# Kernel optimization log

Hardware: AMD Instinct MI355X
Metric: run time of the kernel (lower is better)

Reference implementation:

```python
import jax, jax.numpy as jnp
import numpy as np

N = 100000   # nodes
E = 1600000  # edges (avg degree 16)
DIM = 128    # feature dim
EPS = 1e-6
NEG_SLOPE = 0.2  # tf.nn.leaky_relu default alpha


def layernorm(x, g, b):
    m = jnp.mean(x, axis=-1, keepdims=True)
    v = jnp.mean(jnp.square(x - m), axis=-1, keepdims=True)
    return g * (x - m) * jax.lax.rsqrt(v + EPS) + b


def setup_inputs() -> dict:
    key = jax.random.key(0)
    ks = jax.random.split(key, 12)
    s = 1.0 / np.sqrt(DIM)
    return {
        "query": jax.random.normal(ks[0], (N, DIM), jnp.float32),
        "adj_val": jax.random.uniform(ks[1], (E,), jnp.float32),
        "w_W": jax.random.normal(ks[2], (DIM, DIM), jnp.float32) * s,
        "w_b": jnp.zeros((DIM,), jnp.float32),
        "w1_W": jax.random.normal(ks[3], (DIM, DIM), jnp.float32) * s,
        "w1_b": jnp.zeros((DIM,), jnp.float32),
        "w2_W": jax.random.normal(ks[4], (DIM, DIM), jnp.float32) * s,
        "w2_b": jnp.zeros((DIM,), jnp.float32),
        "ln1_g": jnp.ones((DIM,), jnp.float32),
        "ln1_b": jnp.zeros((DIM,), jnp.float32),
        "ln2_g": jnp.ones((DIM,), jnp.float32),
        "ln2_b": jnp.zeros((DIM,), jnp.float32),
        "adj_row": jnp.sort(jax.random.randint(ks[5], (E,), 0, N, jnp.int32)),
        "adj_col": jax.random.randint(ks[6], (E,), 0, N, jnp.int32),
    }


def reference(query, adj_val, w_W, w_b, w1_W, w1_b, w2_W, w2_b,
              ln1_g, ln1_b, ln2_g, ln2_b, adj_row, adj_col):
    q = layernorm(query, ln1_g, ln1_b)          # [N, D]
    k = q                                        # key is None -> key = query
    value = k @ w_W + w_b                        # [N, D]

    # per-node scalar scores (mean_sum=False branch); dropout in eval mode (identity)
    sum1 = jnp.tanh(jnp.sum(q @ w1_W + w1_b, axis=1))   # [N]
    sum2 = jnp.tanh(jnp.sum(k @ w2_W + w2_b, axis=1))   # [N]

    # sparse add of col-scaled and row-scaled adjacency, then leaky_relu
    logits = jax.nn.leaky_relu(
        adj_val * sum1[adj_row] + adj_val * sum2[adj_col], NEG_SLOPE)  # [E]

    # sparse row-wise softmax over nonzeros
    row_max = jax.ops.segment_max(logits, adj_row, num_segments=N)
    ex = jnp.exp(logits - row_max[adj_row])
    row_sum = jax.ops.segment_sum(ex, adj_row, num_segments=N)
    attn = ex / row_sum[adj_row]                 # [E]

    # spmm: out[i] = sum_e attn[e] * value[col[e]]
    out = jax.ops.segment_sum(attn[:, None] * value[adj_col], adj_row,
                              num_segments=N)    # [N, D]
    return layernorm(out, ln2_g, ln2_b)
```

## Files before the change

### kernel.cpp

```cpp
#include <hip/hip_runtime.h>
#include <hip/hip_bf16.h>

typedef __attribute__((ext_vector_type(8))) short short8;
typedef __attribute__((ext_vector_type(8))) unsigned short ushort8;
typedef __attribute__((ext_vector_type(4))) float f32x4;
typedef __attribute__((ext_vector_type(2))) float f32x2;
typedef __attribute__((ext_vector_type(4))) unsigned int uint4v;

#define DIM 128
#define EPS 1e-6f

__device__ __forceinline__ float wave_sum(float v){
  #pragma unroll
  for (int m = 32; m >= 1; m >>= 1) v += __shfl_xor(v, m);
  return v;
}

__global__ void setup_kernel(const float* __restrict__ w_W,
                             const float* __restrict__ w1_W, const float* __restrict__ w1_b,
                             const float* __restrict__ w2_W, const float* __restrict__ w2_b,
                             __hip_bfloat16* __restrict__ wt_bf,
                             float* __restrict__ u1, float* __restrict__ u2,
                             float* __restrict__ c12){
  const int b = blockIdx.x, tid = threadIdx.x;
  if (b == 0){
    if (tid < DIM){
      float s1 = 0.f, s2 = 0.f;
      for (int j = 0; j < DIM; ++j){ s1 += w1_W[tid*DIM + j]; s2 += w2_W[tid*DIM + j]; }
      u1[tid] = s1; u2[tid] = s2;
    }
    if (tid < 64){
      float c1 = w1_b[tid] + w1_b[tid + 64];
      float c2 = w2_b[tid] + w2_b[tid + 64];
      c1 = wave_sum(c1); c2 = wave_sum(c2);
      if (tid == 0){ c12[0] = c1; c12[1] = c2; }
    }
  } else {
    int idx = (b - 1) * 256 + tid;
    int j = idx >> 7, d = idx & 127;
    wt_bf[idx] = __float2bfloat16(w_W[d*DIM + j]);
  }
}

__launch_bounds__(256)
__global__ void node_kernel(const float* __restrict__ query,
                            const __hip_bfloat16* __restrict__ wt_bf,
                            const float* __restrict__ w_b,
                            const float* __restrict__ ln1_g, const float* __restrict__ ln1_b,
                            const float* __restrict__ u1, const float* __restrict__ u2,
                            const float* __restrict__ c12,
                            unsigned char* __restrict__ value_q,
                            float* __restrict__ sum1, float2* __restrict__ s2v, int N){
  __shared__ __hip_bfloat16 A[64][136];
  const int tid  = threadIdx.x;
  const int lane = tid & 63;
  const int w    = tid >> 6;
  const int q16  = lane >> 4;
  const int lq   = lane & 15;
  const int base = blockIdx.x * 64;

  float uu1[8], uu2[8], gg[8], bv[8];
  {
    const float* p1 = u1 + lq*8; const float* p2 = u2 + lq*8;
    const float* pg = ln1_g + lq*8; const float* pb = ln1_b + lq*8;
    #pragma unroll
    for (int j = 0; j < 8; ++j){ uu1[j]=p1[j]; uu2[j]=p2[j]; gg[j]=pg[j]; bv[j]=pb[j]; }
  }
  const float c1 = c12[0], c2 = c12[1];

  #pragma unroll
  for (int it = 0; it < 4; ++it){
    const int row = w*16 + it*4 + q16;
    const int n   = base + row;
    float x[8];
    if (n < N){
      const float* qp = query + (size_t)n*DIM + lq*8;
      #pragma unroll
      for (int j = 0; j < 8; ++j) x[j] = qp[j];
    } else {
      #pragma unroll
      for (int j = 0; j < 8; ++j) x[j] = 0.f;
    }
    float s = 0.f, s2 = 0.f;
    #pragma unroll
    for (int j = 0; j < 8; ++j){ s += x[j]; s2 += x[j]*x[j]; }
    #pragma unroll
    for (int m = 1; m <= 8; m <<= 1){ s += __shfl_xor(s, m); s2 += __shfl_xor(s2, m); }
    const float mean = s * (1.f/128.f);
    const float var  = s2 * (1.f/128.f) - mean*mean;
    const float rs   = rsqrtf(var + EPS);

    float p1 = 0.f, p2 = 0.f;
    unsigned pk[4];
    #pragma unroll
    for (int j = 0; j < 4; ++j){
      float n0 = gg[2*j]   * (x[2*j]   - mean) * rs + bv[2*j];
      float n1 = gg[2*j+1] * (x[2*j+1] - mean) * rs + bv[2*j+1];
      p1 += n0*uu1[2*j] + n1*uu1[2*j+1];
      p2 += n0*uu2[2*j] + n1*uu2[2*j+1];
      union { __hip_bfloat16 h; unsigned short u; } a_, b_;
      a_.h = __float2bfloat16(n0); b_.h = __float2bfloat16(n1);
      pk[j] = ((unsigned)b_.u << 16) | (unsigned)a_.u;
    }
    uint4v pv = { pk[0], pk[1], pk[2], pk[3] };
    *(uint4v*)&A[row][lq*8] = pv;
    #pragma unroll
    for (int m = 1; m <= 8; m <<= 1){ p1 += __shfl_xor(p1, m); p2 += __shfl_xor(p2, m); }
    if (lq == 0 && n < N){
      sum1[n]   = tanhf(p1 + c1);
      s2v[n].x  = tanhf(p2 + c2);
    }
  }
  __syncthreads();

  const int rh = (w & 1) * 32;
  const int ch = (w >> 1) * 64;
  short8 afr[2][4];
  #pragma unroll
  for (int m = 0; m < 2; ++m)
    #pragma unroll
    for (int ks = 0; ks < 4; ++ks)
      afr[m][ks] = *(const short8*)&A[rh + m*16 + lq][ks*32 + q16*8];
  __syncthreads();

  #pragma unroll
  for (int jj = 0; jj < 4; ++jj){
    const int colb = ch + jj*16;
    f32x4 acc[2];
    acc[0] = (f32x4){0.f,0.f,0.f,0.f};
    acc[1] = (f32x4){0.f,0.f,0.f,0.f};
    #pragma unroll
    for (int ks = 0; ks < 4; ++ks){
      short8 bfr = *(const short8*)(wt_bf + (size_t)(colb + lq)*DIM + ks*32 + q16*8);
      acc[0] = __builtin_amdgcn_mfma_f32_16x16x32_bf16(afr[0][ks], bfr, acc[0], 0, 0, 0);
      acc[1] = __builtin_amdgcn_mfma_f32_16x16x32_bf16(afr[1][ks], bfr, acc[1], 0, 0, 0);
    }
    const int col  = colb + lq;
    const float bias = w_b[col];
    #pragma unroll
    for (int m = 0; m < 2; ++m)
      #pragma unroll
      for (int i = 0; i < 4; ++i)
        A[rh + m*16 + q16*4 + i][col] = __float2bfloat16(acc[m][i] + bias);
  }
  __syncthreads();

  const int row = tid >> 2, seg = tid & 3;
  const int n = base + row;
  float vals[32];
  float amax = 0.f;
  const ushort8* ap = (const ushort8*)&A[row][seg*32];
  #pragma unroll
  for (int h = 0; h < 4; ++h){
    ushort8 vv = ap[h];
    #pragma unroll
    for (int j = 0; j < 8; ++j){
      float f = __uint_as_float((unsigned)vv[j] << 16);
      vals[h*8 + j] = f;
      amax = fmaxf(amax, fabsf(f));
    }
  }
  amax = fmaxf(amax, __shfl_xor(amax, 1));
  amax = fmaxf(amax, __shfl_xor(amax, 2));
  const float qs = amax > 0.f ? 127.f / amax : 0.f;
  if (n < N){
    if (seg == 0) s2v[n].y = amax * (1.f/127.f);
    unsigned dw[8];
    #pragma unroll
    for (int d = 0; d < 8; ++d){
      unsigned q0 = (unsigned)__float2int_rn(fmaf(vals[4*d+0], qs, 128.f));
      unsigned q1 = (unsigned)__float2int_rn(fmaf(vals[4*d+1], qs, 128.f));
      unsigned q2 = (unsigned)__float2int_rn(fmaf(vals[4*d+2], qs, 128.f));
      unsigned q3 = (unsigned)__float2int_rn(fmaf(vals[4*d+3], qs, 128.f));
      dw[d] = q0 | (q1 << 8) | (q2 << 16) | (q3 << 24);
    }
    uint4v* dst = (uint4v*)(value_q + (size_t)n*DIM + seg*32);
    dst[0] = (uint4v){dw[0], dw[1], dw[2], dw[3]};
    dst[1] = (uint4v){dw[4], dw[5], dw[6], dw[7]};
  }
}

__global__ void pack_kernel(const float* __restrict__ adj_val, const int* __restrict__ adj_row,
                            const int* __restrict__ adj_col,
                            const float* __restrict__ sum1, const float2* __restrict__ s2v,
                            float2* __restrict__ excol, int* __restrict__ row_ptr,
                            int N, int E){
  int e = blockIdx.x * 256 + threadIdx.x;
  if (e >= E) return;
  int r  = adj_row[e];
  int rp = (e > 0) ? adj_row[e-1] : -1;
  if (rp != r){
    for (int rr = rp + 1; rr <= r; ++rr) row_ptr[rr] = e;
  }
  if (e == E - 1){
    for (int rr = r + 1; rr <= N; ++rr) row_ptr[rr] = E;
  }
  float av = adj_val[e];
  int c = adj_col[e];
  float2 sv = s2v[c];
  float x = av * (sum1[r] + sv.x);
  float lg = x > 0.f ? x : 0.2f * x;
  excol[e] = make_float2(__expf(lg) * sv.y, __int_as_float(c << 7));
}

__launch_bounds__(256)
__global__ void edge_kernel(const float2* __restrict__ excol, const int* __restrict__ row_ptr,
                            const unsigned char* __restrict__ value_q,
                            const float* __restrict__ ln2_g, const float* __restrict__ ln2_b,
                            float* __restrict__ out, int N){
  const int lane = threadIdx.x & 63;
  const int r = blockIdx.x * 4 + (threadIdx.x >> 6);
  if (r >= N) return;
  const int e0 = row_ptr[r], e1 = row_ptr[r+1];
  const int q  = lane >> 4;
  const int lq = lane & 15;
  const unsigned char* vbase = value_q + lq*8;

  f32x2 acc2[4];
  #pragma unroll
  for (int j = 0; j < 4; ++j) acc2[j] = (f32x2){0.f, 0.f};
  float sumw = 0.f;

  for (int eb = e0 + q; eb < e1; eb += 16){
    #pragma unroll
    for (int t = 0; t < 4; ++t){
      const int e = eb + t*4;
      float2 ecv = (e < e1) ? excol[e] : make_float2(0.f, __int_as_float(0));
      const float wsc = ecv.x;
      const unsigned voff = (unsigned)__float_as_int(ecv.y);
      uint2 v = *(const uint2*)(vbase + voff);
      sumw += wsc;
      f32x2 w2 = { wsc, wsc };
      f32x2 p0 = { (float)( v.x        & 0xff), (float)((v.x >>  8) & 0xff) };
      f32x2 p1 = { (float)((v.x >> 16) & 0xff), (float)( v.x >> 24)         };
      f32x2 p2 = { (float)( v.y        & 0xff), (float)((v.y >>  8) & 0xff) };
      f32x2 p3 = { (float)((v.y >> 16) & 0xff), (float)( v.y >> 24)         };
      acc2[0] += w2 * p0;
      acc2[1] += w2 * p1;
      acc2[2] += w2 * p2;
      acc2[3] += w2 * p3;
    }
  }

  #pragma unroll
  for (int j = 0; j < 4; ++j){
    acc2[j].x += __shfl_xor(acc2[j].x, 16); acc2[j].y += __shfl_xor(acc2[j].y, 16);
    acc2[j].x += __shfl_xor(acc2[j].x, 32); acc2[j].y += __shfl_xor(acc2[j].y, 32);
  }
  sumw += __shfl_xor(sumw, 16);
  sumw += __shfl_xor(sumw, 32);

  const float bias = 128.f * sumw;
  #pragma unroll
  for (int j = 0; j < 4; ++j){ acc2[j].x -= bias; acc2[j].y -= bias; }

  float sx = 0.f, sxx = 0.f;
  #pragma unroll
  for (int j = 0; j < 4; ++j){
    sx  += acc2[j].x + acc2[j].y;
    sxx += acc2[j].x*acc2[j].x + acc2[j].y*acc2[j].y;
  }
  #pragma unroll
  for (int m = 1; m <= 8; m <<= 1){ sx += __shfl_xor(sx, m); sxx += __shfl_xor(sxx, m); }
  const float mean = sx * (1.f/128.f);
  const float var  = sxx * (1.f/128.f) - mean*mean;
  const float rs   = rsqrtf(var + EPS);

  if (q == 0){
    float4 g0 = ((const float4*)ln2_g)[lq*2], g1 = ((const float4*)ln2_g)[lq*2+1];
    float4 b0 = ((const float4*)ln2_b)[lq*2], b1 = ((const float4*)ln2_b)[lq*2+1];
    float4 o0, o1;
    o0.x = g0.x*(acc2[0].x-mean)*rs + b0.x; o0.y = g0.y*(acc2[0].y-mean)*rs + b0.y;
    o0.z = g0.z*(acc2[1].x-mean)*rs + b0.z; o0.w = g0.w*(acc2[1].y-mean)*rs + b0.w;
    o1.x = g1.x*(acc2[2].x-mean)*rs + b1.x; o1.y = g1.y*(acc2[2].y-mean)*rs + b1.y;
    o1.z = g1.z*(acc2[3].x-mean)*rs + b1.z; o1.w = g1.w*(acc2[3].y-mean)*rs + b1.w;
    float4* op = (float4*)(out + (size_t)r*DIM + lq*8);
    op[0] = o0; op[1] = o1;
  }
}

extern "C" void kernel_launch(void* const* d_in, const int* in_sizes, int n_in,
                              void* d_out, int out_size, void* d_ws, size_t ws_size,
                              hipStream_t stream){
  const float* query   = (const float*)d_in[0];
  const float* adj_val = (const float*)d_in[1];
  const float* w_W     = (const float*)d_in[2];
  const float* w_b     = (const float*)d_in[3];
  const float* w1_W    = (const float*)d_in[4];
  const float* w1_b    = (const float*)d_in[5];
  const float* w2_W    = (const float*)d_in[6];
  const float* w2_b    = (const float*)d_in[7];
  const float* ln1_g   = (const float*)d_in[8];
  const float* ln1_b   = (const float*)d_in[9];
  const float* ln2_g   = (const float*)d_in[10];
  const float* ln2_b   = (const float*)d_in[11];
  const int*   adj_row = (const int*)d_in[12];
  const int*   adj_col = (const int*)d_in[13];

  const int N = in_sizes[0] / DIM;
  const int E = in_sizes[1];

  char* ws = (char*)d_ws;
  size_t off = 0;
  unsigned char* value_q = (unsigned char*)(ws + off); off += (size_t)N * DIM;
  float* sum1   = (float*)(ws + off); off += (size_t)N * 4;
  float2* s2v   = (float2*)(ws + off); off += (size_t)N * 8;
  int* row_ptr  = (int*)(ws + off);   off += (size_t)(N + 2) * 4;
  float* u1     = (float*)(ws + off); off += DIM * 4;
  float* u2     = (float*)(ws + off); off += DIM * 4;
  float* c12    = (float*)(ws + off); off += 2 * 4;
  off = (off + 63) & ~(size_t)63;
  __hip_bfloat16* wt_bf = (__hip_bfloat16*)(ws + off); off += DIM * DIM * 2;
  off = (off + 63) & ~(size_t)63;
  float2* excol = (float2*)(ws + off);

  setup_kernel<<<65, 256, 0, stream>>>(w_W, w1_W, w1_b, w2_W, w2_b, wt_bf, u1, u2, c12);
  node_kernel<<<(N + 63) / 64, 256, 0, stream>>>(query, wt_bf, w_b, ln1_g, ln1_b,
                                                 u1, u2, c12, value_q, sum1, s2v, N);
  pack_kernel<<<(E + 255) / 256, 256, 0, stream>>>(adj_val, adj_row, adj_col,
                                                   sum1, s2v, excol, row_ptr, N, E);
  edge_kernel<<<(N + 3) / 4, 256, 0, stream>>>(excol, row_ptr, value_q,
                                               ln2_g, ln2_b, (float*)d_out, N);
}
```

Measured before the change: 106.4 us.

## Vectorize loads across kernels, pack two edges per thread, drop redundant bias

The weight row-sum setup now splits each row over two threads using float4 loads and combines the halves through shared memory. node_kernel issues all four query rows' loads up front as float4 pairs. pack_kernel processes two edges per thread with vector loads and one float4 store, reusing sum1 when both edges share a row. edge_kernel reads row_ptr as an int2, splits the edge loop into a full-chunk body plus a guarded tail, and drops the per-row 128*sumw bias correction, since the final layernorm removes any constant shift. Together these aim to cut memory instructions, bounds checks and ALU work, at the cost of more register pressure and relying on layernorm invariance.

```diff
diff --git a/kernel.cpp b/kernel.cpp
--- a/kernel.cpp
+++ b/kernel.cpp
@@ -24,11 +24,19 @@
                              float* __restrict__ c12){
   const int b = blockIdx.x, tid = threadIdx.x;
   if (b == 0){
-    if (tid < DIM){
-      float s1 = 0.f, s2 = 0.f;
-      for (int j = 0; j < DIM; ++j){ s1 += w1_W[tid*DIM + j]; s2 += w2_W[tid*DIM + j]; }
-      u1[tid] = s1; u2[tid] = s2;
-    }
+    __shared__ float p1s[256], p2s[256];
+    const int d = tid & 127, half = tid >> 7;
+    const float4* w1p = (const float4*)(w1_W + d*DIM + half*64);
+    const float4* w2p = (const float4*)(w2_W + d*DIM + half*64);
+    float s1 = 0.f, s2 = 0.f;
+    #pragma unroll 4
+    for (int j = 0; j < 16; ++j){
+      float4 a = w1p[j]; s1 += (a.x + a.y) + (a.z + a.w);
+      float4 c = w2p[j]; s2 += (c.x + c.y) + (c.z + c.w);
+    }
+    p1s[tid] = s1; p2s[tid] = s2;
+    __syncthreads();
+    if (tid < 128){ u1[tid] = p1s[tid] + p1s[tid+128]; u2[tid] = p2s[tid] + p2s[tid+128]; }
     if (tid < 64){
       float c1 = w1_b[tid] + w1_b[tid + 64];
       float c2 = w2_b[tid] + w2_b[tid + 64];
@@ -68,22 +76,28 @@
   }
   const float c1 = c12[0], c2 = c12[1];
 
+  float x[4][8];
+  #pragma unroll
+  for (int it = 0; it < 4; ++it){
+    const int n = base + w*16 + it*4 + q16;
+    if (n < N){
+      const float4* qp = (const float4*)(query + (size_t)n*DIM + lq*8);
+      float4 a = qp[0], b = qp[1];
+      x[it][0]=a.x; x[it][1]=a.y; x[it][2]=a.z; x[it][3]=a.w;
+      x[it][4]=b.x; x[it][5]=b.y; x[it][6]=b.z; x[it][7]=b.w;
+    } else {
+      #pragma unroll
+      for (int j = 0; j < 8; ++j) x[it][j] = 0.f;
+    }
+  }
+
   #pragma unroll
   for (int it = 0; it < 4; ++it){
     const int row = w*16 + it*4 + q16;
     const int n   = base + row;
-    float x[8];
-    if (n < N){
-      const float* qp = query + (size_t)n*DIM + lq*8;
-      #pragma unroll
-      for (int j = 0; j < 8; ++j) x[j] = qp[j];
-    } else {
-      #pragma unroll
-      for (int j = 0; j < 8; ++j) x[j] = 0.f;
-    }
     float s = 0.f, s2 = 0.f;
     #pragma unroll
-    for (int j = 0; j < 8; ++j){ s += x[j]; s2 += x[j]*x[j]; }
+    for (int j = 0; j < 8; ++j){ s += x[it][j]; s2 += x[it][j]*x[it][j]; }
     #pragma unroll
     for (int m = 1; m <= 8; m <<= 1){ s += __shfl_xor(s, m); s2 += __shfl_xor(s2, m); }
     const float mean = s * (1.f/128.f);
@@ -94,8 +108,8 @@
     unsigned pk[4];
     #pragma unroll
     for (int j = 0; j < 4; ++j){
-      float n0 = gg[2*j]   * (x[2*j]   - mean) * rs + bv[2*j];
-      float n1 = gg[2*j+1] * (x[2*j+1] - mean) * rs + bv[2*j+1];
+      float n0 = gg[2*j]   * (x[it][2*j]   - mean) * rs + bv[2*j];
+      float n1 = gg[2*j+1] * (x[it][2*j+1] - mean) * rs + bv[2*j+1];
       p1 += n0*uu1[2*j] + n1*uu1[2*j+1];
       p2 += n0*uu2[2*j] + n1*uu2[2*j+1];
       union { __hip_bfloat16 h; unsigned short u; } a_, b_;
@@ -185,22 +199,37 @@
                             const float* __restrict__ sum1, const float2* __restrict__ s2v,
                             float2* __restrict__ excol, int* __restrict__ row_ptr,
                             int N, int E){
-  int e = blockIdx.x * 256 + threadIdx.x;
-  if (e >= E) return;
-  int r  = adj_row[e];
-  int rp = (e > 0) ? adj_row[e-1] : -1;
-  if (rp != r){
-    for (int rr = rp + 1; rr <= r; ++rr) row_ptr[rr] = e;
-  }
-  if (e == E - 1){
-    for (int rr = r + 1; rr <= N; ++rr) row_ptr[rr] = E;
-  }
-  float av = adj_val[e];
-  int c = adj_col[e];
-  float2 sv = s2v[c];
-  float x = av * (sum1[r] + sv.x);
-  float lg = x > 0.f ? x : 0.2f * x;
-  excol[e] = make_float2(__expf(lg) * sv.y, __int_as_float(c << 7));
+  const int e2 = (blockIdx.x * 256 + threadIdx.x) * 2;
+  if (e2 >= E) return;
+  const int2 rr = *(const int2*)(adj_row + e2);
+  const int rp = (e2 > 0) ? adj_row[e2 - 1] : -1;
+  if (rp != rr.x)
+    for (int t = rp + 1; t <= rr.x; ++t) row_ptr[t] = e2;
+
+  const float2 av = *(const float2*)(adj_val + e2);
+  const int2   cc = *(const int2*)(adj_col + e2);
+  const float2 sv0 = s2v[cc.x];
+  const float s10 = sum1[rr.x];
+
+  float x0 = av.x * (s10 + sv0.x);
+  float l0 = x0 > 0.f ? x0 : 0.2f * x0;
+  float2 ec0 = make_float2(__expf(l0) * sv0.y, __int_as_float(cc.x << 7));
+
+  if (e2 + 1 < E){
+    if (rr.y != rr.x)
+      for (int t = rr.x + 1; t <= rr.y; ++t) row_ptr[t] = e2 + 1;
+    const float2 sv1 = s2v[cc.y];
+    const float s11 = (rr.y == rr.x) ? s10 : sum1[rr.y];
+    float x1 = av.y * (s11 + sv1.x);
+    float l1 = x1 > 0.f ? x1 : 0.2f * x1;
+    float2 ec1 = make_float2(__expf(l1) * sv1.y, __int_as_float(cc.y << 7));
+    *(float4*)(excol + e2) = make_float4(ec0.x, ec0.y, ec1.x, ec1.y);
+    if (e2 + 1 == E - 1)
+      for (int t = rr.y + 1; t <= N; ++t) row_ptr[t] = E;
+  } else {
+    excol[e2] = ec0;
+    for (int t = rr.x + 1; t <= N; ++t) row_ptr[t] = E;
+  }
 }
 
 __launch_bounds__(256)
@@ -211,7 +240,8 @@
   const int lane = threadIdx.x & 63;
   const int r = blockIdx.x * 4 + (threadIdx.x >> 6);
   if (r >= N) return;
-  const int e0 = row_ptr[r], e1 = row_ptr[r+1];
+  const int2 rp = *(const int2*)(row_ptr + r);
+  const int e0 = rp.x, e1 = rp.y;
   const int q  = lane >> 4;
   const int lq = lane & 15;
   const unsigned char* vbase = value_q + lq*8;
@@ -219,17 +249,15 @@
   f32x2 acc2[4];
   #pragma unroll
   for (int j = 0; j < 4; ++j) acc2[j] = (f32x2){0.f, 0.f};
-  float sumw = 0.f;
-
-  for (int eb = e0 + q; eb < e1; eb += 16){
+
+  int sb = e0;
+  for (; sb + 16 <= e1; sb += 16){
     #pragma unroll
     for (int t = 0; t < 4; ++t){
-      const int e = eb + t*4;
-      float2 ecv = (e < e1) ? excol[e] : make_float2(0.f, __int_as_float(0));
+      float2 ecv = excol[sb + q + t*4];
       const float wsc = ecv.x;
       const unsigned voff = (unsigned)__float_as_int(ecv.y);
       uint2 v = *(const uint2*)(vbase + voff);
-      sumw += wsc;
       f32x2 w2 = { wsc, wsc };
       f32x2 p0 = { (float)( v.x        & 0xff), (float)((v.x >>  8) & 0xff) };
       f32x2 p1 = { (float)((v.x >> 16) & 0xff), (float)( v.x >> 24)         };
@@ -241,18 +269,31 @@
       acc2[3] += w2 * p3;
     }
   }
+  if (sb < e1){
+    #pragma unroll
+    for (int t = 0; t < 4; ++t){
+      const int e = sb + q + t*4;
+      float2 ecv = (e < e1) ? excol[e] : make_float2(0.f, 0.f);
+      const float wsc = ecv.x;
+      const unsigned voff = (unsigned)__float_as_int(ecv.y);
+      uint2 v = *(const uint2*)(vbase + voff);
+      f32x2 w2 = { wsc, wsc };
+      f32x2 p0 = { (float)( v.x        & 0xff), (float)((v.x >>  8) & 0xff) };
+      f32x2 p1 = { (float)((v.x >> 16) & 0xff), (float)( v.x >> 24)         };
+      f32x2 p2 = { (float)( v.y        & 0xff), (float)((v.y >>  8) & 0xff) };
+      f32x2 p3 = { (float)((v.y >> 16) & 0xff), (float)( v.y >> 24)         };
+      acc2[0] += w2 * p0;
+      acc2[1] += w2 * p1;
+      acc2[2] += w2 * p2;
+      acc2[3] += w2 * p3;
+    }
+  }
 
   #pragma unroll
   for (int j = 0; j < 4; ++j){
     acc2[j].x += __shfl_xor(acc2[j].x, 16); acc2[j].y += __shfl_xor(acc2[j].y, 16);
     acc2[j].x += __shfl_xor(acc2[j].x, 32); acc2[j].y += __shfl_xor(acc2[j].y, 32);
   }
-  sumw += __shfl_xor(sumw, 16);
-  sumw += __shfl_xor(sumw, 32);
-
-  const float bias = 128.f * sumw;
-  #pragma unroll
-  for (int j = 0; j < 4; ++j){ acc2[j].x -= bias; acc2[j].y -= bias; }
 
   float sx = 0.f, sxx = 0.f;
   #pragma unroll
@@ -317,8 +358,8 @@
   setup_kernel<<<65, 256, 0, stream>>>(w_W, w1_W, w1_b, w2_W, w2_b, wt_bf, u1, u2, c12);
   node_kernel<<<(N + 63) / 64, 256, 0, stream>>>(query, wt_bf, w_b, ln1_g, ln1_b,
                                                  u1, u2, c12, value_q, sum1, s2v, N);
-  pack_kernel<<<(E + 255) / 256, 256, 0, stream>>>(adj_val, adj_row, adj_col,
-                                                   sum1, s2v, excol, row_ptr, N, E);
+  pack_kernel<<<(E/2 + 255) / 256, 256, 0, stream>>>(adj_val, adj_row, adj_col,
+                                                     sum1, s2v, excol, row_ptr, N, E);
   edge_kernel<<<(N + 3) / 4, 256, 0, stream>>>(excol, row_ptr, value_q,
                                                ln2_g, ln2_b, (float*)d_out, N);
 }
```

Measured after the change: 105.6 us. No clear change (-0.8%).
